# Optimization experiments

Measured on AMD Instinct MI355X. Metric: run time of the kernel, lower is better.

The kernel has to match this reference:

```python
import jax, jax.numpy as jnp
import numpy as np

N_NODES = 50000
N_EDGES = 1600000
IN_DIM = 128
HID = 128
N_GRAPHS = 64
N_CLASSES = 1


def _seg_sum(x, ids, n):
    return jax.ops.segment_sum(x, ids, num_segments=n)


def _gcn_layer(h, W, b, src, dst, src_isqrt, dst_isqrt):
    # DGL GraphConv, norm='both': D_dst^{-1/2} A D_src^{-1/2} (h W) + b
    hw = h @ W                                  # [N, out]
    msg = (hw * src_isqrt[:, None])[src]        # gather -> [E, out]
    agg = _seg_sum(msg, dst, h.shape[0])        # scatter-add -> [N, out]
    return agg * dst_isqrt[:, None] + b


def setup_inputs() -> dict:
    key = jax.random.key(0)
    ks = jax.random.split(key, 16)
    x = jax.random.normal(ks[0], (N_NODES, IN_DIM), dtype=jnp.float32)
    src = jax.random.randint(ks[1], (N_EDGES,), 0, N_NODES)
    dst = jax.random.randint(ks[2], (N_EDGES,), 0, N_NODES)
    graph_id = jnp.sort(jax.random.randint(ks[3], (N_NODES,), 0, N_GRAPHS))
    s = 1.0 / np.sqrt(HID)
    params = {
        'W1': jax.random.uniform(ks[4], (IN_DIM, HID), jnp.float32, -s, s),
        'b1': jnp.zeros((HID,), jnp.float32),
        'W2': jax.random.uniform(ks[5], (HID, HID), jnp.float32, -s, s),
        'b2': jnp.zeros((HID,), jnp.float32),
        'Wc1': jax.random.uniform(ks[6], (HID, HID // 2), jnp.float32, -s, s),
        'bc1': jnp.zeros((HID // 2,), jnp.float32),
        'Wc2': jax.random.uniform(ks[7], (HID // 2, HID // 4), jnp.float32, -s, s),
        'bc2': jnp.zeros((HID // 4,), jnp.float32),
        'Wc3': jax.random.uniform(ks[8], (HID // 4, HID // 8), jnp.float32, -s, s),
        'bc3': jnp.zeros((HID // 8,), jnp.float32),
        'Wc4': jax.random.uniform(ks[9], (HID // 8, N_CLASSES), jnp.float32, -s, s),
        'bc4': jnp.zeros((N_CLASSES,), jnp.float32),
    }
    return dict(x=x, src=src, dst=dst, graph_id=graph_id, num_graphs=N_GRAPHS, **params)


def reference(x, src, dst, graph_id, num_graphs, W1, b1, W2, b2,
              Wc1, bc1, Wc2, bc2, Wc3, bc3, Wc4, bc4):
    n = x.shape[0]
    ones = jnp.ones((src.shape[0],), x.dtype)
    out_deg = jnp.clip(_seg_sum(ones, src, n), 1.0)
    in_deg = jnp.clip(_seg_sum(ones, dst, n), 1.0)
    src_isqrt = jax.lax.rsqrt(out_deg)
    dst_isqrt = jax.lax.rsqrt(in_deg)

    h = jax.nn.relu(_gcn_layer(x, W1, b1, src, dst, src_isqrt, dst_isqrt))
    h = jax.nn.relu(_gcn_layer(h, W2, b2, src, dst, src_isqrt, dst_isqrt))

    # dgl.mean_nodes: per-graph mean of node features
    sums = _seg_sum(h, graph_id, num_graphs)                       # [G, HID]
    cnts = jnp.clip(_seg_sum(jnp.ones((n,), h.dtype), graph_id, num_graphs), 1.0)
    hg = sums / cnts[:, None]

    o = jax.nn.relu(hg @ Wc1 + bc1)
    o = jax.nn.relu(o @ Wc2 + bc2)
    o = jax.nn.relu(o @ Wc3 + bc3)
    return o @ Wc4 + bc4
```

## Files before the change

### kernel.cpp

```cpp
#include <hip/hip_runtime.h>
#include <hip/hip_fp16.h>

#define FDIM 128
#define NGRAPH 64
#define POOL_CHUNK 64
#define CBLK 256
#define OCHUNK 12800
#define OBLK 64

typedef _Float16 f16;
typedef f16 f16x8 __attribute__((ext_vector_type(8)));
typedef float f32x4 __attribute__((ext_vector_type(4)));
typedef float f32x2 __attribute__((ext_vector_type(2)));

__device__ __forceinline__ int lower_bound_i(const int* a, int n, int v) {
    int lo = 0, hi = n;
    while (lo < hi) { int m = (lo + hi) >> 1; if (a[m] < v) lo = m + 1; else hi = m; }
    return lo;
}

__global__ __launch_bounds__(256) void k_pre(
        const float* __restrict__ W1, f16* __restrict__ W1h, f16* __restrict__ W1l,
        const float* __restrict__ W2, f16* __restrict__ W2h, f16* __restrict__ W2l,
        float* __restrict__ hg, const int* __restrict__ dst, int* __restrict__ partial,
        int E, int NBIN, int CE4) {
    __shared__ int lds[4 * 257];
    const int t = threadIdx.x;
    int b = blockIdx.x;
    if (b < 128) {
        int i = b * 256 + t;
        if (i < NGRAPH * FDIM) hg[i] = 0.f;
        int j = i & 16383;
        int k = j >> 7, n = j & 127;
        const float* W = (i < 16384) ? W1 : W2;
        f16* Wh = (i < 16384) ? W1h : W2h;
        f16* Wl = (i < 16384) ? W1l : W2l;
        float v = W[j];
        f16 hi = (f16)v;
        Wh[n * FDIM + k] = hi;
        Wl[n * FDIM + k] = (f16)(v - (float)hi);
    } else {
        b -= 128;
        for (int i = t; i < 4 * 257; i += 256) lds[i] = 0;
        __syncthreads();
        const int wv = t >> 6;
        int* hh = &lds[wv * 257];
        const int s = b * CE4, e = min(E, s + CE4);
        for (int i = s + t * 4; i < e; i += 1024) {
            if (i + 4 <= e) {
                uint4 d4 = *(const uint4*)&dst[i];
                atomicAdd(&hh[d4.x >> 8], 1);
                atomicAdd(&hh[d4.y >> 8], 1);
                atomicAdd(&hh[d4.z >> 8], 1);
                atomicAdd(&hh[d4.w >> 8], 1);
            } else {
                for (int j = i; j < e; j++) atomicAdd(&hh[dst[j] >> 8], 1);
            }
        }
        __syncthreads();
        for (int i = t; i < NBIN; i += 256)
            partial[i * CBLK + b] = lds[i] + lds[257 + i] + lds[514 + i] + lds[771 + i];
    }
}

__global__ __launch_bounds__(256) void k_scan_oh(
        const int* __restrict__ partial, int* __restrict__ offs, int* __restrict__ bsum,
        int M, const int* __restrict__ src, int* __restrict__ out_part,
        int E, int N, int NBIN) {
    __shared__ int lds[OCHUNK];
    const int t = threadIdx.x;
    int b = blockIdx.x;
    if (b < NBIN) {
        int i = b * 256 + t;
        int v = (i < M) ? partial[i] : 0;
        lds[t] = v;
        __syncthreads();
        for (int off = 1; off < 256; off <<= 1) {
            int x = (t >= off) ? lds[t - off] : 0;
            __syncthreads();
            lds[t] += x;
            __syncthreads();
        }
        if (i < M) offs[i] = lds[t] - v;
        if (t == 255) bsum[b] = lds[t];
    } else {
        b -= NBIN;
        const int c = b / OBLK, sl = b % OBLK;
        for (int i = t; i < OCHUNK; i += 256) lds[i] = 0;
        __syncthreads();
        const int lo = c * OCHUNK;
        const int SE = (E + OBLK - 1) / OBLK;
        const int s = sl * SE, e = min(E, s + SE);
        for (int i = s + t * 4; i < e; i += 1024) {
            if (i + 4 <= e) {
                uint4 s4 = *(const uint4*)&src[i];
                int v0 = (int)s4.x - lo, v1 = (int)s4.y - lo;
                int v2 = (int)s4.z - lo, v3 = (int)s4.w - lo;
                if ((unsigned)v0 < (unsigned)OCHUNK) atomicAdd(&lds[v0], 1);
                if ((unsigned)v1 < (unsigned)OCHUNK) atomicAdd(&lds[v1], 1);
                if ((unsigned)v2 < (unsigned)OCHUNK) atomicAdd(&lds[v2], 1);
                if ((unsigned)v3 < (unsigned)OCHUNK) atomicAdd(&lds[v3], 1);
            } else {
                for (int j = i; j < e; j++) {
                    int v = src[j] - lo;
                    if ((unsigned)v < (unsigned)OCHUNK) atomicAdd(&lds[v], 1);
                }
            }
        }
        __syncthreads();
        const int hi = min(N - lo, OCHUNK);
        for (int i = t; i < hi; i += 256)
            out_part[(size_t)sl * N + lo + i] = lds[i];
    }
}

__global__ __launch_bounds__(256) void k_coarse_scatter(
        const int* __restrict__ src, const int* __restrict__ dst,
        const int* __restrict__ offs, const int* __restrict__ bsum,
        unsigned* __restrict__ coarse_buf, int E, int CE4, int NBIN) {
    __shared__ int cur[256], sb[256];
    const int t = threadIdx.x, b = blockIdx.x;
    int v = (t < NBIN) ? bsum[t] : 0;
    sb[t] = v;
    __syncthreads();
    for (int off = 1; off < 256; off <<= 1) {
        int x = (t >= off) ? sb[t - off] : 0;
        __syncthreads();
        sb[t] += x;
        __syncthreads();
    }
    if (t < NBIN) cur[t] = offs[t * CBLK + b] + (sb[t] - v);
    __syncthreads();
    const int s = b * CE4, e = min(E, s + CE4);
    for (int i = s + t * 4; i < e; i += 1024) {
        if (i + 4 <= e) {
            uint4 d4 = *(const uint4*)&dst[i];
            uint4 s4 = *(const uint4*)&src[i];
            int p0 = atomicAdd(&cur[d4.x >> 8], 1);
            int p1 = atomicAdd(&cur[d4.y >> 8], 1);
            int p2 = atomicAdd(&cur[d4.z >> 8], 1);
            int p3 = atomicAdd(&cur[d4.w >> 8], 1);
            coarse_buf[p0] = (d4.x << 16) | s4.x;
            coarse_buf[p1] = (d4.y << 16) | s4.y;
            coarse_buf[p2] = (d4.z << 16) | s4.z;
            coarse_buf[p3] = (d4.w << 16) | s4.w;
        } else {
            for (int j = i; j < e; j++) {
                unsigned d = (unsigned)dst[j];
                int p = atomicAdd(&cur[d >> 8], 1);
                coarse_buf[p] = (d << 16) | (unsigned)src[j];
            }
        }
    }
}

template<bool IN_F16>
__device__ __forceinline__ void gemm_body(
        f16* smem, float* sisql, int blk,
        const void* __restrict__ Xv, const f16* __restrict__ Wh,
        const f16* __restrict__ Wl, const int* __restrict__ out_part,
        float* __restrict__ sisq, unsigned char* __restrict__ out, int N) {
    const int t = threadIdx.x;
    const int w = t >> 6;
    const int lane = t & 63;
    const int base = blk * 128;

    if (t < 128) {
        int row = base + t;
        float sv = 1.f;
        if (row < N) {
            if (IN_F16) {
                sv = sisq[row];
            } else {
                int a = 0;
#pragma unroll
                for (int bb = 0; bb < OBLK; bb++) a += out_part[(size_t)bb * N + row];
                sv = rsqrtf((float)max(a, 1));
                sisq[row] = sv;
            }
        }
        sisql[t] = sv;
    }
    for (int i = t; i < 2048; i += 256) {
        int n = i >> 4, kc = (i & 15) * 8;
        *(uint4*)&smem[n * 136 + kc] = *(const uint4*)&Wh[n * FDIM + kc];
    }
    __syncthreads();

    const int mrow = lane & 15;
    const int kq = (lane >> 4) * 8;
    const int arow0 = min(base + w * 32 + mrow, N - 1);
    const int arow1 = min(base + w * 32 + 16 + mrow, N - 1);

    f16x8 a0[4], a1[4];
    if (IN_F16) {
        const f16* X = (const f16*)Xv;
#pragma unroll
        for (int kk = 0; kk < 4; kk++) {
            a0[kk] = *(const f16x8*)&X[(size_t)arow0 * FDIM + kk * 32 + kq];
            a1[kk] = *(const f16x8*)&X[(size_t)arow1 * FDIM + kk * 32 + kq];
        }
    } else {
        const float* X = (const float*)Xv;
#pragma unroll
        for (int kk = 0; kk < 4; kk++) {
            float4 u0 = *(const float4*)&X[(size_t)arow0 * FDIM + kk * 32 + kq];
            float4 u1 = *(const float4*)&X[(size_t)arow0 * FDIM + kk * 32 + kq + 4];
            float4 v0 = *(const float4*)&X[(size_t)arow1 * FDIM + kk * 32 + kq];
            float4 v1 = *(const float4*)&X[(size_t)arow1 * FDIM + kk * 32 + kq + 4];
            f16x8 av;
            av[0] = (f16)u0.x; av[1] = (f16)u0.y; av[2] = (f16)u0.z; av[3] = (f16)u0.w;
            av[4] = (f16)u1.x; av[5] = (f16)u1.y; av[6] = (f16)u1.z; av[7] = (f16)u1.w;
            a0[kk] = av;
            av[0] = (f16)v0.x; av[1] = (f16)v0.y; av[2] = (f16)v0.z; av[3] = (f16)v0.w;
            av[4] = (f16)v1.x; av[5] = (f16)v1.y; av[6] = (f16)v1.z; av[7] = (f16)v1.w;
            a1[kk] = av;
        }
    }

    f32x4 acc0[8], acc1[8];
#pragma unroll
    for (int nt = 0; nt < 8; nt++) {
        acc0[nt] = (f32x4){0.f, 0.f, 0.f, 0.f};
        acc1[nt] = (f32x4){0.f, 0.f, 0.f, 0.f};
    }

#pragma unroll
    for (int kk = 0; kk < 4; kk++) {
#pragma unroll
        for (int nt = 0; nt < 8; nt++) {
            f16x8 bh = *(const f16x8*)&smem[(nt * 16 + mrow) * 136 + kk * 32 + kq];
            f16x8 bl = *(const f16x8*)&Wl[(nt * 16 + mrow) * FDIM + kk * 32 + kq];
            acc0[nt] = __builtin_amdgcn_mfma_f32_16x16x32_f16(a0[kk], bh, acc0[nt], 0, 0, 0);
            acc1[nt] = __builtin_amdgcn_mfma_f32_16x16x32_f16(a1[kk], bh, acc1[nt], 0, 0, 0);
            acc0[nt] = __builtin_amdgcn_mfma_f32_16x16x32_f16(a0[kk], bl, acc0[nt], 0, 0, 0);
            acc1[nt] = __builtin_amdgcn_mfma_f32_16x16x32_f16(a1[kk], bl, acc1[nt], 0, 0, 0);
        }
    }

    const int r0 = (lane >> 4) * 4;
    float sv0[4], sv1[4];
#pragma unroll
    for (int j = 0; j < 4; j++) {
        sv0[j] = sisql[w * 32 + r0 + j];
        sv1[j] = sisql[w * 32 + 16 + r0 + j];
    }
    __syncthreads();
#pragma unroll
    for (int nt = 0; nt < 8; nt++) {
        int c = nt * 16 + mrow;
#pragma unroll
        for (int j = 0; j < 4; j++) {
            smem[(w * 32 + r0 + j) * 136 + c]      = (f16)(acc0[nt][j] * sv0[j]);
            smem[(w * 32 + 16 + r0 + j) * 136 + c] = (f16)(acc1[nt][j] * sv1[j]);
        }
    }
    __syncthreads();
    {
        int r = t >> 1, cb = (t & 1) * 64;
        int row = base + r;
        if (row < N) {
            unsigned char* dstp = out + (size_t)row * FDIM + cb;
#pragma unroll
            for (int g2 = 0; g2 < 4; g2++) {
                unsigned wv[4];
#pragma unroll
                for (int k2 = 0; k2 < 4; k2++) {
                    const f16* p = &smem[r * 136 + cb + g2 * 16 + k2 * 4];
                    int w0 = __builtin_amdgcn_cvt_pk_fp8_f32((float)p[0], (float)p[1], 0, false);
                    w0 = __builtin_amdgcn_cvt_pk_fp8_f32((float)p[2], (float)p[3], w0, true);
                    wv[k2] = (unsigned)w0;
                }
                uint4 u;
                u.x = wv[0]; u.y = wv[1]; u.z = wv[2]; u.w = wv[3];
                *(uint4*)&dstp[g2 * 16] = u;
            }
        }
    }
}

__global__ __launch_bounds__(256) void k_fine_gemm(
        const unsigned* __restrict__ coarse_buf, const int* __restrict__ bsum,
        int* __restrict__ csr_src, int* __restrict__ row_ptr, int N, int E, int NBIN,
        const float* __restrict__ x, const f16* __restrict__ Wh,
        const f16* __restrict__ Wl, const int* __restrict__ out_part,
        float* __restrict__ sisq, unsigned char* __restrict__ hws) {
    __shared__ __align__(16) f16 smem[128 * 136];
    __shared__ float sisql[128];
    const int t = threadIdx.x;
    const int g = blockIdx.x;
    if (g >= NBIN) {
        gemm_body<false>(smem, sisql, g - NBIN, x, Wh, Wl, out_part, sisq, hws, N);
        return;
    }
    int* h  = (int*)smem;
    int* sc = h + 256;
    int* cur = h + 512;
    int bv = (t < NBIN) ? bsum[t] : 0;
    sc[t] = bv;
    __syncthreads();
    for (int off = 1; off < 256; off <<= 1) {
        int xx = (t >= off) ? sc[t - off] : 0;
        __syncthreads();
        sc[t] += xx;
        __syncthreads();
    }
    __syncthreads();
    if (t == 0) { h[0] = sc[g] - bsum[g]; h[1] = sc[g]; }
    __syncthreads();
    const int s = h[0], e = h[1];
    __syncthreads();
    h[t] = 0;
    __syncthreads();
    for (int i = s + t; i < e; i += 256)
        atomicAdd(&h[(coarse_buf[i] >> 16) & 255], 1);
    __syncthreads();
    int v = h[t];
    sc[t] = v;
    __syncthreads();
    for (int off = 1; off < 256; off <<= 1) {
        int xx = (t >= off) ? sc[t - off] : 0;
        __syncthreads();
        sc[t] += xx;
        __syncthreads();
    }
    const int excl = sc[t] - v;
    const int node = g * 256 + t;
    if (node < N) row_ptr[node] = s + excl;
    if (node == N) row_ptr[N] = s + excl;
    cur[t] = s + excl;
    __syncthreads();
    for (int i = s + t; i < e; i += 256) {
        unsigned p = coarse_buf[i];
        int f = (p >> 16) & 255;
        int pos = atomicAdd(&cur[f], 1);
        csr_src[pos] = (int)(p & 0xFFFFu);
    }
    if (g == NBIN - 1 && t == 0 && (N & 255) == 0) row_ptr[N] = E;
}

__global__ __launch_bounds__(256) void k_gemm2(
        const f16* __restrict__ X, const f16* __restrict__ Wh,
        const f16* __restrict__ Wl, float* __restrict__ sisq,
        unsigned char* __restrict__ out, int N) {
    __shared__ __align__(16) f16 smem[128 * 136];
    __shared__ float sisql[128];
    gemm_body<true>(smem, sisql, blockIdx.x, X, Wh, Wl, nullptr, sisq, out, N);
}

__device__ __forceinline__ void accF8(float* acc, uint2 v) {
    f32x2 a0 = __builtin_amdgcn_cvt_pk_f32_fp8((int)v.x, false);
    f32x2 a1 = __builtin_amdgcn_cvt_pk_f32_fp8((int)v.x, true);
    f32x2 a2 = __builtin_amdgcn_cvt_pk_f32_fp8((int)v.y, false);
    f32x2 a3 = __builtin_amdgcn_cvt_pk_f32_fp8((int)v.y, true);
    acc[0] += a0.x; acc[1] += a0.y; acc[2] += a1.x; acc[3] += a1.y;
    acc[4] += a2.x; acc[5] += a2.y; acc[6] += a3.x; acc[7] += a3.y;
}

__global__ __launch_bounds__(256) void k_aggregate(
        const unsigned char* __restrict__ hws, const int* __restrict__ csr_src,
        const int* __restrict__ row_ptr,
        const float* __restrict__ bias, f16* __restrict__ out, int N) {
    const int t = threadIdx.x;
    const int node = blockIdx.x * 16 + (t >> 4);
    if (node >= N) return;
    const int fbase = (t & 15) * 8;

    const int s = row_ptr[node];
    const int e = row_ptr[node + 1];
    float acc[8];
#pragma unroll
    for (int j = 0; j < 8; j++) acc[j] = 0.f;

    int i = s;
    for (; i + 8 <= e; i += 8) {
        int u[8];
#pragma unroll
        for (int j = 0; j < 8; j++) u[j] = csr_src[i + j];
        uint2 v[8];
#pragma unroll
        for (int j = 0; j < 8; j++)
            v[j] = *(const uint2*)(hws + (size_t)u[j] * FDIM + fbase);
#pragma unroll
        for (int j = 0; j < 8; j++) accF8(acc, v[j]);
    }
    if (i + 4 <= e) {
        int u[4];
#pragma unroll
        for (int j = 0; j < 4; j++) u[j] = csr_src[i + j];
        uint2 v[4];
#pragma unroll
        for (int j = 0; j < 4; j++)
            v[j] = *(const uint2*)(hws + (size_t)u[j] * FDIM + fbase);
#pragma unroll
        for (int j = 0; j < 4; j++) accF8(acc, v[j]);
        i += 4;
    }
    for (; i < e; i++) {
        int u = csr_src[i];
        uint2 v = *(const uint2*)(hws + (size_t)u * FDIM + fbase);
        accF8(acc, v);
    }

    const float d = rsqrtf((float)max(e - s, 1));
    f16 res[8];
#pragma unroll
    for (int j = 0; j < 8; j++)
        res[j] = (f16)fmaxf(fmaf(acc[j], d, bias[fbase + j]), 0.f);
    *(uint4*)(out + (size_t)node * FDIM + fbase) = *(const uint4*)res;
}

__global__ void k_pool_sum(const f16* __restrict__ h, const int* __restrict__ gid,
                           float* __restrict__ hg, int N) {
    const int t = threadIdx.x;
    int s = blockIdx.x * POOL_CHUNK;
    int e = min(N, s + POOL_CHUNK);
    if (s >= e) return;
    int g = gid[s];
    float acc = 0.f;
    for (int n = s; n < e; n++) {
        int gn = gid[n];
        if (gn != g) {
            atomicAdd(&hg[g * FDIM + t], acc);
            acc = 0.f;
            g = gn;
        }
        acc += (float)h[(size_t)n * FDIM + t];
    }
    atomicAdd(&hg[g * FDIM + t], acc);
}

__global__ __launch_bounds__(256) void k_mlp(
        const float* __restrict__ hg, const int* __restrict__ gid, int N,
        const float* __restrict__ Wc1, const float* __restrict__ bc1,
        const float* __restrict__ Wc2, const float* __restrict__ bc2,
        const float* __restrict__ Wc3, const float* __restrict__ bc3,
        const float* __restrict__ Wc4, const float* __restrict__ bc4,
        float* __restrict__ out) {
    __shared__ float A[NGRAPH * 128];
    __shared__ float O1[NGRAPH * 64];
    __shared__ float O2[NGRAPH * 32];
    __shared__ float O3[NGRAPH * 16];
    __shared__ float inv_cnt[NGRAPH];
    const int t = threadIdx.x;

    if (t < NGRAPH) {
        int s = lower_bound_i(gid, N, t);
        int e = lower_bound_i(gid, N, t + 1);
        inv_cnt[t] = 1.f / fmaxf((float)(e - s), 1.f);
    }
    __syncthreads();

    for (int i = t; i < NGRAPH * 128; i += 256) A[i] = hg[i] * inv_cnt[i >> 7];
    __syncthreads();

    for (int i = t; i < NGRAPH * 64; i += 256) {
        int g = i >> 6, o = i & 63;
        float a = bc1[o];
        for (int k = 0; k < 128; k++) a = fmaf(A[g * 128 + k], Wc1[k * 64 + o], a);
        O1[i] = fmaxf(a, 0.f);
    }
    __syncthreads();

    for (int i = t; i < NGRAPH * 32; i += 256) {
        int g = i >> 5, o = i & 31;
        float a = bc2[o];
        for (int k = 0; k < 64; k++) a = fmaf(O1[g * 64 + k], Wc2[k * 32 + o], a);
        O2[i] = fmaxf(a, 0.f);
    }
    __syncthreads();

    for (int i = t; i < NGRAPH * 16; i += 256) {
        int g = i >> 4, o = i & 15;
        float a = bc3[o];
        for (int k = 0; k < 32; k++) a = fmaf(O2[g * 32 + k], Wc3[k * 16 + o], a);
        O3[i] = fmaxf(a, 0.f);
    }
    __syncthreads();

    if (t < NGRAPH) {
        float a = bc4[0];
        for (int k = 0; k < 16; k++) a = fmaf(O3[t * 16 + k], Wc4[k], a);
        out[t] = a;
    }
}

extern "C" void kernel_launch(void* const* d_in, const int* in_sizes, int n_in,
                              void* d_out, int out_size, void* d_ws, size_t ws_size,
                              hipStream_t stream) {
    const float* x   = (const float*)d_in[0];
    const int*   src = (const int*)d_in[1];
    const int*   dst = (const int*)d_in[2];
    const int*   gid = (const int*)d_in[3];
    const float* W1  = (const float*)d_in[5];
    const float* b1  = (const float*)d_in[6];
    const float* W2  = (const float*)d_in[7];
    const float* b2  = (const float*)d_in[8];
    const float* Wc1 = (const float*)d_in[9];
    const float* bc1 = (const float*)d_in[10];
    const float* Wc2 = (const float*)d_in[11];
    const float* bc2 = (const float*)d_in[12];
    const float* Wc3 = (const float*)d_in[13];
    const float* bc3 = (const float*)d_in[14];
    const float* Wc4 = (const float*)d_in[15];
    const float* bc4 = (const float*)d_in[16];
    float* out = (float*)d_out;

    const int N = in_sizes[0] / FDIM;
    const int E = in_sizes[1];

    const int NBIN = (N + 255) >> 8;
    const int M    = NBIN * CBLK;
    const int CE4  = (((E + CBLK - 1) / CBLK) + 3) & ~3;
    const int OC   = (N + OCHUNK - 1) / OCHUNK;

    char* w = (char*)d_ws;
    size_t off = 0;
    auto alloc = [&](size_t bytes) -> void* {
        void* p = w + off;
        off = (off + bytes + 255) & ~(size_t)255;
        return p;
    };
    unsigned char* hws = (unsigned char*)alloc((size_t)N * FDIM);
    f16*   h       = (f16*)   alloc((size_t)N * FDIM * 2);
    int*   csr_src = (int*)   alloc((size_t)E * 4);
    unsigned* coarse_buf = (unsigned*)alloc((size_t)E * 4);
    int*   out_part = (int*) alloc((size_t)OBLK * N * 4);
    int*   partial = (int*)   alloc((size_t)M * 4);
    int*   offs    = (int*)   alloc((size_t)M * 4);
    int*   row_ptr = (int*)   alloc((size_t)(N + 1) * 4);
    float* sisq    = (float*) alloc((size_t)N * 4);
    int*   bsum    = (int*)   alloc(256 * 4);
    float* hg      = (float*) alloc(NGRAPH * FDIM * 4);
    f16*   W1t     = (f16*)   alloc(FDIM * FDIM * 2);
    f16*   W1l     = (f16*)   alloc(FDIM * FDIM * 2);
    f16*   W2t     = (f16*)   alloc(FDIM * FDIM * 2);
    f16*   W2l     = (f16*)   alloc(FDIM * FDIM * 2);

    const int gT = (N + 127) / 128;
    const int gA = (N + 15) / 16;

    k_pre<<<128 + CBLK, 256, 0, stream>>>(
        W1, W1t, W1l, W2, W2t, W2l, hg, dst, partial, E, NBIN, CE4);
    k_scan_oh<<<NBIN + OC * OBLK, 256, 0, stream>>>(
        partial, offs, bsum, M, src, out_part, E, N, NBIN);
    k_coarse_scatter<<<CBLK, 256, 0, stream>>>(src, dst, offs, bsum, coarse_buf, E, CE4, NBIN);
    k_fine_gemm<<<NBIN + gT, 256, 0, stream>>>(
        coarse_buf, bsum, csr_src, row_ptr, N, E, NBIN,
        x, W1t, W1l, out_part, sisq, hws);
    k_aggregate<<<gA, 256, 0, stream>>>(hws, csr_src, row_ptr, b1, h, N);
    k_gemm2<<<gT, 256, 0, stream>>>(h, W2t, W2l, sisq, hws, N);
    k_aggregate<<<gA, 256, 0, stream>>>(hws, csr_src, row_ptr, b2, h, N);
    const int gP = (N + POOL_CHUNK - 1) / POOL_CHUNK;
    k_pool_sum<<<gP, 128, 0, stream>>>(h, gid, hg, N);
    k_mlp<<<1, 256, 0, stream>>>(hg, gid, N, Wc1, bc1, Wc2, bc2, Wc3, bc3, Wc4, bc4, out);
}
```

Baseline: 288.1 us.

## Compute out-degree via global atomics in k_pre and fuse mean-pool into aggregation

Replaces the separate LDS-histogram out-degree pass (64 partial slices per node summed in the GEMM) with global atomicAdds on a single out_deg array inside the existing dst-binning kernel, after a memset. It also folds the per-graph pooling into the second aggregation, accumulating relu outputs into a small shared per-block graph table and then into hg, so the final h is never written or re-read and k_pool_sum is dropped. The cost is 1.6M global atomics contending on random addresses, one extra launch for the memset, and float atomic accumulation order becoming nondeterministic.

Measured after the change: 341.8 us. 18.6% more time.

```diff
diff --git a/kernel.cpp b/kernel.cpp
--- a/kernel.cpp
+++ b/kernel.cpp
@@ -3,10 +3,7 @@
 
 #define FDIM 128
 #define NGRAPH 64
-#define POOL_CHUNK 64
 #define CBLK 256
-#define OCHUNK 12800
-#define OBLK 64
 
 typedef _Float16 f16;
 typedef f16 f16x8 __attribute__((ext_vector_type(8)));
@@ -22,7 +19,8 @@
 __global__ __launch_bounds__(256) void k_pre(
         const float* __restrict__ W1, f16* __restrict__ W1h, f16* __restrict__ W1l,
         const float* __restrict__ W2, f16* __restrict__ W2h, f16* __restrict__ W2l,
-        float* __restrict__ hg, const int* __restrict__ dst, int* __restrict__ partial,
+        float* __restrict__ hg, const int* __restrict__ src, const int* __restrict__ dst,
+        int* __restrict__ out_deg, int* __restrict__ partial,
         int E, int NBIN, int CE4) {
     __shared__ int lds[4 * 257];
     const int t = threadIdx.x;
@@ -49,12 +47,20 @@
         for (int i = s + t * 4; i < e; i += 1024) {
             if (i + 4 <= e) {
                 uint4 d4 = *(const uint4*)&dst[i];
+                uint4 s4 = *(const uint4*)&src[i];
                 atomicAdd(&hh[d4.x >> 8], 1);
                 atomicAdd(&hh[d4.y >> 8], 1);
                 atomicAdd(&hh[d4.z >> 8], 1);
                 atomicAdd(&hh[d4.w >> 8], 1);
+                atomicAdd(&out_deg[s4.x], 1);
+                atomicAdd(&out_deg[s4.y], 1);
+                atomicAdd(&out_deg[s4.z], 1);
+                atomicAdd(&out_deg[s4.w], 1);
             } else {
-                for (int j = i; j < e; j++) atomicAdd(&hh[dst[j] >> 8], 1);
+                for (int j = i; j < e; j++) {
+                    atomicAdd(&hh[dst[j] >> 8], 1);
+                    atomicAdd(&out_deg[src[j]], 1);
+                }
             }
         }
         __syncthreads();
@@ -63,55 +69,24 @@
     }
 }
 
-__global__ __launch_bounds__(256) void k_scan_oh(
+__global__ __launch_bounds__(256) void k_scan(
         const int* __restrict__ partial, int* __restrict__ offs, int* __restrict__ bsum,
-        int M, const int* __restrict__ src, int* __restrict__ out_part,
-        int E, int N, int NBIN) {
-    __shared__ int lds[OCHUNK];
+        int M) {
+    __shared__ int lds[256];
     const int t = threadIdx.x;
-    int b = blockIdx.x;
-    if (b < NBIN) {
-        int i = b * 256 + t;
-        int v = (i < M) ? partial[i] : 0;
-        lds[t] = v;
-        __syncthreads();
-        for (int off = 1; off < 256; off <<= 1) {
-            int x = (t >= off) ? lds[t - off] : 0;
-            __syncthreads();
-            lds[t] += x;
-            __syncthreads();
-        }
-        if (i < M) offs[i] = lds[t] - v;
-        if (t == 255) bsum[b] = lds[t];
-    } else {
-        b -= NBIN;
-        const int c = b / OBLK, sl = b % OBLK;
-        for (int i = t; i < OCHUNK; i += 256) lds[i] = 0;
-        __syncthreads();
-        const int lo = c * OCHUNK;
-        const int SE = (E + OBLK - 1) / OBLK;
-        const int s = sl * SE, e = min(E, s + SE);
-        for (int i = s + t * 4; i < e; i += 1024) {
-            if (i + 4 <= e) {
-                uint4 s4 = *(const uint4*)&src[i];
-                int v0 = (int)s4.x - lo, v1 = (int)s4.y - lo;
-                int v2 = (int)s4.z - lo, v3 = (int)s4.w - lo;
-                if ((unsigned)v0 < (unsigned)OCHUNK) atomicAdd(&lds[v0], 1);
-                if ((unsigned)v1 < (unsigned)OCHUNK) atomicAdd(&lds[v1], 1);
-                if ((unsigned)v2 < (unsigned)OCHUNK) atomicAdd(&lds[v2], 1);
-                if ((unsigned)v3 < (unsigned)OCHUNK) atomicAdd(&lds[v3], 1);
-            } else {
-                for (int j = i; j < e; j++) {
-                    int v = src[j] - lo;
-                    if ((unsigned)v < (unsigned)OCHUNK) atomicAdd(&lds[v], 1);
-                }
-            }
-        }
-        __syncthreads();
-        const int hi = min(N - lo, OCHUNK);
-        for (int i = t; i < hi; i += 256)
-            out_part[(size_t)sl * N + lo + i] = lds[i];
-    }
+    const int b = blockIdx.x;
+    int i = b * 256 + t;
+    int v = (i < M) ? partial[i] : 0;
+    lds[t] = v;
+    __syncthreads();
+    for (int off = 1; off < 256; off <<= 1) {
+        int x = (t >= off) ? lds[t - off] : 0;
+        __syncthreads();
+        lds[t] += x;
+        __syncthreads();
+    }
+    if (i < M) offs[i] = lds[t] - v;
+    if (t == 255) bsum[b] = lds[t];
 }
 
 __global__ __launch_bounds__(256) void k_coarse_scatter(
@@ -158,7 +133,7 @@
 __device__ __forceinline__ void gemm_body(
         f16* smem, float* sisql, int blk,
         const void* __restrict__ Xv, const f16* __restrict__ Wh,
-        const f16* __restrict__ Wl, const int* __restrict__ out_part,
+        const f16* __restrict__ Wl, const int* __restrict__ out_deg,
         float* __restrict__ sisq, unsigned char* __restrict__ out, int N) {
     const int t = threadIdx.x;
     const int w = t >> 6;
@@ -172,10 +147,7 @@
             if (IN_F16) {
                 sv = sisq[row];
             } else {
-                int a = 0;
-#pragma unroll
-                for (int bb = 0; bb < OBLK; bb++) a += out_part[(size_t)bb * N + row];
-                sv = rsqrtf((float)max(a, 1));
+                sv = rsqrtf((float)max(out_deg[row], 1));
                 sisq[row] = sv;
             }
         }
@@ -283,14 +255,14 @@
         const unsigned* __restrict__ coarse_buf, const int* __restrict__ bsum,
         int* __restrict__ csr_src, int* __restrict__ row_ptr, int N, int E, int NBIN,
         const float* __restrict__ x, const f16* __restrict__ Wh,
-        const f16* __restrict__ Wl, const int* __restrict__ out_part,
+        const f16* __restrict__ Wl, const int* __restrict__ out_deg,
         float* __restrict__ sisq, unsigned char* __restrict__ hws) {
     __shared__ __align__(16) f16 smem[128 * 136];
     __shared__ float sisql[128];
     const int t = threadIdx.x;
     const int g = blockIdx.x;
     if (g >= NBIN) {
-        gemm_body<false>(smem, sisql, g - NBIN, x, Wh, Wl, out_part, sisq, hws, N);
+        gemm_body<false>(smem, sisql, g - NBIN, x, Wh, Wl, out_deg, sisq, hws, N);
         return;
     }
     int* h  = (int*)smem;
@@ -357,17 +329,18 @@
     acc[4] += a2.x; acc[5] += a2.y; acc[6] += a3.x; acc[7] += a3.y;
 }
 
+template<bool POOL>
 __global__ __launch_bounds__(256) void k_aggregate(
         const unsigned char* __restrict__ hws, const int* __restrict__ csr_src,
         const int* __restrict__ row_ptr,
-        const float* __restrict__ bias, f16* __restrict__ out, int N) {
+        const float* __restrict__ bias, f16* __restrict__ out,
+        const int* __restrict__ gid, float* __restrict__ hg, int N) {
     const int t = threadIdx.x;
     const int node = blockIdx.x * 16 + (t >> 4);
-    if (node >= N) return;
     const int fbase = (t & 15) * 8;
 
-    const int s = row_ptr[node];
-    const int e = row_ptr[node + 1];
+    int s = 0, e = 0;
+    if (node < N) { s = row_ptr[node]; e = row_ptr[node + 1]; }
     float acc[8];
 #pragma unroll
     for (int j = 0; j < 8; j++) acc[j] = 0.f;
@@ -403,31 +376,45 @@
     }
 
     const float d = rsqrtf((float)max(e - s, 1));
-    f16 res[8];
+    float res[8];
 #pragma unroll
     for (int j = 0; j < 8; j++)
-        res[j] = (f16)fmaxf(fmaf(acc[j], d, bias[fbase + j]), 0.f);
-    *(uint4*)(out + (size_t)node * FDIM + fbase) = *(const uint4*)res;
-}
-
-__global__ void k_pool_sum(const f16* __restrict__ h, const int* __restrict__ gid,
-                           float* __restrict__ hg, int N) {
-    const int t = threadIdx.x;
-    int s = blockIdx.x * POOL_CHUNK;
-    int e = min(N, s + POOL_CHUNK);
-    if (s >= e) return;
-    int g = gid[s];
-    float acc = 0.f;
-    for (int n = s; n < e; n++) {
-        int gn = gid[n];
-        if (gn != g) {
-            atomicAdd(&hg[g * FDIM + t], acc);
-            acc = 0.f;
-            g = gn;
-        }
-        acc += (float)h[(size_t)n * FDIM + t];
-    }
-    atomicAdd(&hg[g * FDIM + t], acc);
+        res[j] = fmaxf(fmaf(acc[j], d, bias[fbase + j]), 0.f);
+
+    if (!POOL) {
+        if (node < N) {
+            f16 r16[8];
+#pragma unroll
+            for (int j = 0; j < 8; j++) r16[j] = (f16)res[j];
+            *(uint4*)(out + (size_t)node * FDIM + fbase) = *(const uint4*)r16;
+        }
+    } else {
+        __shared__ float hgl[8 * 128];
+        const int nfirst = blockIdx.x * 16;
+        const int nlast = min(nfirst + 15, N - 1);
+        const int g0 = gid[nfirst];
+        const int span = gid[nlast] - g0 + 1;
+        if (span <= 8) {
+            for (int k = t; k < span * 128; k += 256) hgl[k] = 0.f;
+            __syncthreads();
+            if (node < N) {
+                const int gg = gid[node] - g0;
+#pragma unroll
+                for (int j = 0; j < 8; j++)
+                    atomicAdd(&hgl[gg * 128 + fbase + j], res[j]);
+            }
+            __syncthreads();
+            for (int k = t; k < span * 128; k += 256)
+                atomicAdd(&hg[g0 * 128 + k], hgl[k]);
+        } else {
+            if (node < N) {
+                const int gg = gid[node];
+#pragma unroll
+                for (int j = 0; j < 8; j++)
+                    atomicAdd(&hg[gg * 128 + fbase + j], res[j]);
+            }
+        }
+    }
 }
 
 __global__ __launch_bounds__(256) void k_mlp(
@@ -512,7 +499,6 @@
     const int NBIN = (N + 255) >> 8;
     const int M    = NBIN * CBLK;
     const int CE4  = (((E + CBLK - 1) / CBLK) + 3) & ~3;
-    const int OC   = (N + OCHUNK - 1) / OCHUNK;
 
     char* w = (char*)d_ws;
     size_t off = 0;
@@ -525,7 +511,7 @@
     f16*   h       = (f16*)   alloc((size_t)N * FDIM * 2);
     int*   csr_src = (int*)   alloc((size_t)E * 4);
     unsigned* coarse_buf = (unsigned*)alloc((size_t)E * 4);
-    int*   out_part = (int*) alloc((size_t)OBLK * N * 4);
+    int*   out_deg = (int*)   alloc((size_t)N * 4);
     int*   partial = (int*)   alloc((size_t)M * 4);
     int*   offs    = (int*)   alloc((size_t)M * 4);
     int*   row_ptr = (int*)   alloc((size_t)(N + 1) * 4);
@@ -540,18 +526,16 @@
     const int gT = (N + 127) / 128;
     const int gA = (N + 15) / 16;
 
+    hipMemsetAsync(out_deg, 0, (size_t)N * 4, stream);
     k_pre<<<128 + CBLK, 256, 0, stream>>>(
-        W1, W1t, W1l, W2, W2t, W2l, hg, dst, partial, E, NBIN, CE4);
-    k_scan_oh<<<NBIN + OC * OBLK, 256, 0, stream>>>(
-        partial, offs, bsum, M, src, out_part, E, N, NBIN);
+        W1, W1t, W1l, W2, W2t, W2l, hg, src, dst, out_deg, partial, E, NBIN, CE4);
+    k_scan<<<NBIN, 256, 0, stream>>>(partial, offs, bsum, M);
     k_coarse_scatter<<<CBLK, 256, 0, stream>>>(src, dst, offs, bsum, coarse_buf, E, CE4, NBIN);
     k_fine_gemm<<<NBIN + gT, 256, 0, stream>>>(
         coarse_buf, bsum, csr_src, row_ptr, N, E, NBIN,
-        x, W1t, W1l, out_part, sisq, hws);
-    k_aggregate<<<gA, 256, 0, stream>>>(hws, csr_src, row_ptr, b1, h, N);
+        x, W1t, W1l, out_deg, sisq, hws);
+    k_aggregate<false><<<gA, 256, 0, stream>>>(hws, csr_src, row_ptr, b1, h, nullptr, nullptr, N);
     k_gemm2<<<gT, 256, 0, stream>>>(h, W2t, W2l, sisq, hws, N);
-    k_aggregate<<<gA, 256, 0, stream>>>(hws, csr_src, row_ptr, b2, h, N);
-    const int gP = (N + POOL_CHUNK - 1) / POOL_CHUNK;
-    k_pool_sum<<<gP, 128, 0, stream>>>(h, gid, hg, N);
+    k_aggregate<true><<<gA, 256, 0, stream>>>(hws, csr_src, row_ptr, b2, nullptr, gid, hg, N);
     k_mlp<<<1, 256, 0, stream>>>(hg, gid, N, Wc1, bc1, Wc2, bc2, Wc3, bc3, Wc4, bc4, out);
 }
```
